# Performance work log

Hardware: AMD Instinct MI355X
Metric: run time of the kernel (lower is better)

## Reference

```python
import jax, jax.numpy as jnp
import numpy as np

B, N, D, E, H = 4, 2048, 512, 16, 1024
CAP = max(4, min(N, int(N * 2.0 / E)))   # eval capacity_factor = 2.0 -> 256
EPS = 1e-9
THRESH = 0.2  # second_threshold_eval


def setup_inputs() -> dict:
    key = jax.random.key(0)
    ks = jax.random.split(key, 10)
    f32 = jnp.float32
    return {
        "X": jax.random.normal(ks[0], (B, N, D), f32),
        "probs": jax.random.uniform(ks[1], (B, N), f32),
        "W1": jax.random.normal(ks[2], (D, D), f32) * (1.0 / np.sqrt(D)),
        "b1": jnp.zeros((D,), f32),
        "Wg": jax.random.normal(ks[3], (D, E), f32),  # Top2Gating uses randn init
        "We1": jax.random.normal(ks[4], (E, D, H), f32) * (1.0 / np.sqrt(D)),
        "We2": jax.random.normal(ks[5], (E, H, D), f32) * (1.0 / np.sqrt(H)),
        "W3": jax.random.normal(ks[6], (D, 4), f32) * (1.0 / np.sqrt(D)),
        "b3": jnp.zeros((4,), f32),
        "W4": jax.random.normal(ks[7], (4, 1), f32) * 0.5,
        "b4": jnp.zeros((1,), f32),
    }


def top2_gating(x, Wg, probs):
    # x: [B, N, D] -> raw gates [B, N, E]
    raw = jax.nn.softmax(jnp.einsum('bnd,de->bne', x, Wg), axis=-1)
    dt = raw.dtype

    gate1 = jnp.max(raw, axis=-1)
    idx1 = jnp.argmax(raw, axis=-1)
    mask1 = jax.nn.one_hot(idx1, E, dtype=dt)
    density_proxy = raw

    raw_wo1 = raw * (1.0 - mask1)
    gate2 = jnp.max(raw_wo1, axis=-1)
    idx2 = jnp.argmax(raw_wo1, axis=-1)
    mask2 = jax.nn.one_hot(idx2, E, dtype=dt)

    denom = gate1 + gate2 + EPS
    gate1 = gate1 / denom
    gate2 = gate2 / denom

    # load-balancing loss (computed but wrapper discards it)
    density1 = jnp.mean(mask1, axis=-2)
    loss = jnp.mean(jnp.mean(density_proxy, axis=-2) * density1) * float(E ** 2)

    # second policy == 'random'
    mask2 = mask2 * (probs < (gate2 / max(THRESH, EPS))).astype(dt)[..., None]

    # exclusive cumsum along the group dim gives position within each expert
    pos1 = (jnp.cumsum(mask1, axis=-2) - mask1) * mask1          # [B, N, E]
    mask1 = mask1 * (pos1 < float(CAP)).astype(dt)
    mask1_count = jnp.sum(mask1, axis=-2, keepdims=True)
    mask1_flat = jnp.sum(mask1, axis=-1)                          # [B, N]
    pos1_flat = jnp.sum(pos1, axis=-1)
    gate1 = gate1 * mask1_flat

    pos2 = ((jnp.cumsum(mask2, axis=-2) - mask2) + mask1_count) * mask2
    mask2 = mask2 * (pos2 < float(CAP)).astype(dt)
    mask2_flat = jnp.sum(mask2, axis=-1)
    pos2_flat = jnp.sum(pos2, axis=-1)
    gate2 = gate2 * mask2_flat

    # safe one-hot: out-of-range positions map to all-zeros (jax.nn.one_hot semantics)
    oh_p1 = jax.nn.one_hot(pos1_flat.astype(jnp.int32), CAP, dtype=dt)
    oh_p2 = jax.nn.one_hot(pos2_flat.astype(jnp.int32), CAP, dtype=dt)
    oh_e1 = jax.nn.one_hot(idx1, E, dtype=dt)
    oh_e2 = jax.nn.one_hot(idx2, E, dtype=dt)

    combine = ((gate1 * mask1_flat)[..., None, None] * oh_e1[..., :, None] * oh_p1[..., None, :]
               + (gate2 * mask2_flat)[..., None, None] * oh_e2[..., :, None] * oh_p2[..., None, :])
    dispatch = (combine != 0).astype(dt)
    return dispatch, combine, loss


def reference(X, probs, W1, b1, Wg, We1, We2, W3, b3, W4, b4):
    h = X @ W1 + b1                                              # linear1
    dispatch, combine, loss = top2_gating(h, Wg, probs)
    exp_in = jnp.einsum('bnd,bnec->ebcd', h, dispatch)           # dispatch
    hid = jax.nn.leaky_relu(jnp.einsum('ebcd,edh->ebch', exp_in, We1))
    exp_out = jnp.einsum('ebch,ehd->ebcd', hid, We2)             # experts
    moe_out = jnp.einsum('bnec,ebcd->bnd', combine, exp_out)     # combine
    out = (moe_out @ W3 + b3) @ W4 + b4                          # hidden3 -> act3
    return out
```

## Files before the change

kernel.cpp:

```cpp
#include <hip/hip_runtime.h>
#include <hip/hip_bf16.h>

#define NB 4
#define NN 2048
#define ND 512
#define NE 16
#define NH 1024
#define CAP 256
#define NTOK (NB*NN)

typedef __attribute__((ext_vector_type(8))) short bf16x8;
typedef __attribute__((ext_vector_type(4))) float f32x4;
typedef __attribute__((ext_vector_type(8))) unsigned short u16x8;

__device__ __forceinline__ void gload16(const void* gsrc, void* lds) {
    __builtin_amdgcn_global_load_lds((const __attribute__((address_space(1))) void*)gsrc,
                                     (__attribute__((address_space(3))) void*)lds, 16, 0, 0);
}
__device__ __forceinline__ unsigned short f2bf(float f) {
    union { __hip_bfloat16 b; unsigned short u; } v; v.b = __float2bfloat16(f); return v.u;
}

__global__ __launch_bounds__(256) void prep_w_kernel(const float* __restrict__ W1,
                                                     const float* __restrict__ Wg,
                                                     unsigned short* __restrict__ W1B,
                                                     float* __restrict__ WcT,
                                                     float* __restrict__ zbuf) {
    const int tid = threadIdx.x;
    int bid = blockIdx.x;
    if (bid < 128) {
        if (bid == 0) zbuf[tid] = 0.f;
        const int w = tid >> 6, l = tid & 63;
        const int d = bid * 4 + w;
        float a0 = 0.f, a1 = 0.f, a2 = 0.f, a3 = 0.f, a4 = 0.f, a5 = 0.f, a6 = 0.f, a7 = 0.f;
        float a8 = 0.f, a9 = 0.f, aA = 0.f, aB = 0.f, aC = 0.f, aD = 0.f, aE = 0.f, aF = 0.f;
        #pragma unroll
        for (int ch = 0; ch < 8; ++ch) {
            float x = W1[(size_t)d * ND + ch * 64 + l];
            const float4* wg4 = (const float4*)(Wg + (size_t)(ch * 64 + l) * NE);
            float4 g0 = wg4[0], g1 = wg4[1], g2 = wg4[2], g3 = wg4[3];
            a0 = fmaf(x, g0.x, a0); a1 = fmaf(x, g0.y, a1); a2 = fmaf(x, g0.z, a2); a3 = fmaf(x, g0.w, a3);
            a4 = fmaf(x, g1.x, a4); a5 = fmaf(x, g1.y, a5); a6 = fmaf(x, g1.z, a6); a7 = fmaf(x, g1.w, a7);
            a8 = fmaf(x, g2.x, a8); a9 = fmaf(x, g2.y, a9); aA = fmaf(x, g2.z, aA); aB = fmaf(x, g2.w, aB);
            aC = fmaf(x, g3.x, aC); aD = fmaf(x, g3.y, aD); aE = fmaf(x, g3.z, aE); aF = fmaf(x, g3.w, aF);
        }
        float accs[16] = {a0, a1, a2, a3, a4, a5, a6, a7, a8, a9, aA, aB, aC, aD, aE, aF};
        #pragma unroll
        for (int off = 32; off >= 1; off >>= 1)
            #pragma unroll
            for (int e = 0; e < 16; ++e) accs[e] += __shfl_xor(accs[e], off);
        #pragma unroll
        for (int e = 0; e < 16; ++e)
            if (l == e) WcT[e * ND + d] = accs[e];
        return;
    }
    bid -= 128;
    {
        int dblk = bid >> 1, hblk = bid & 1;
        const float* src = W1 + (size_t)(dblk * 64) * ND + hblk * 256 + tid;
        unsigned short* dst = W1B + (size_t)(dblk * 512 + hblk * 256 + tid) * 64;
        float v[64];
        #pragma unroll
        for (int j = 0; j < 64; ++j) v[j] = src[(size_t)j * ND];
        #pragma unroll
        for (int q = 0; q < 8; ++q) {
            u16x8 o;
            #pragma unroll
            for (int j = 0; j < 8; ++j) o[j] = f2bf(v[q * 8 + j]);
            *(u16x8*)(dst + q * 8) = o;
        }
    }
}

__global__ __launch_bounds__(256) void gating_stream_kernel(const float* __restrict__ X,
                                                            const float* __restrict__ WcT,
                                                            const float* __restrict__ probs,
                                                            const float* __restrict__ b3,
                                                            const float* __restrict__ W4,
                                                            const float* __restrict__ b4,
                                                            const float* __restrict__ We1,
                                                            unsigned short* __restrict__ Xbf,
                                                            unsigned short* __restrict__ We1B,
                                                            int* __restrict__ idx1a, int* __restrict__ idx2a,
                                                            float* __restrict__ g1a, float* __restrict__ g2a,
                                                            float* __restrict__ out) {
    __shared__ float wc[NE * ND];
    const int tid = threadIdx.x;
    int bid = blockIdx.x;
    const int w = tid >> 6, l = tid & 63;
    if (bid < 512) {
        #pragma unroll
        for (int i = 0; i < 32; ++i) wc[tid + 256 * i] = WcT[tid + 256 * i];
        float c0v = b4[0];
        #pragma unroll
        for (int j = 0; j < 4; ++j) c0v += b3[j] * W4[j];
        __syncthreads();
        const float4* wc4 = (const float4*)wc;
        for (int j = 0; j < 4; ++j) {
            int tok = bid * 16 + j * 4 + w;
            const float4* xrow = (const float4*)(X + (size_t)tok * ND);
            float4 x0 = xrow[l], x1 = xrow[l + 64];
            {
                ushort4 o0, o1;
                o0.x = f2bf(x0.x); o0.y = f2bf(x0.y); o0.z = f2bf(x0.z); o0.w = f2bf(x0.w);
                o1.x = f2bf(x1.x); o1.y = f2bf(x1.y); o1.z = f2bf(x1.z); o1.w = f2bf(x1.w);
                *(ushort4*)(Xbf + (size_t)tok * ND + 4 * l) = o0;
                *(ushort4*)(Xbf + (size_t)tok * ND + 256 + 4 * l) = o1;
            }
            float acc[NE];
            #pragma unroll
            for (int e = 0; e < NE; ++e) {
                float4 w0 = wc4[e * 128 + l], w1 = wc4[e * 128 + l + 64];
                acc[e] = x0.x * w0.x + x0.y * w0.y + x0.z * w0.z + x0.w * w0.w
                       + x1.x * w1.x + x1.y * w1.y + x1.z * w1.z + x1.w * w1.w;
            }
            #pragma unroll
            for (int off = 32; off >= 1; off >>= 1)
                #pragma unroll
                for (int e = 0; e < NE; ++e) acc[e] += __shfl_xor(acc[e], off);

            if (l == 0) {
                float m = acc[0];
                #pragma unroll
                for (int e = 1; e < NE; ++e) m = fmaxf(m, acc[e]);
                float s = 0.f;
                #pragma unroll
                for (int e = 0; e < NE; ++e) { acc[e] = expf(acc[e] - m); s += acc[e]; }
                float inv = 1.f / s;
                #pragma unroll
                for (int e = 0; e < NE; ++e) acc[e] *= inv;
                int i1 = 0; float g1 = acc[0];
                #pragma unroll
                for (int e = 1; e < NE; ++e) if (acc[e] > g1) { g1 = acc[e]; i1 = e; }
                int i2 = -1; float g2 = -1.f;
                #pragma unroll
                for (int e = 0; e < NE; ++e) if (e != i1 && acc[e] > g2) { g2 = acc[e]; i2 = e; }
                float denom = g1 + g2 + 1e-9f;
                float g1n = g1 / denom, g2n = g2 / denom;
                bool flag = probs[tok] < (g2n / 0.2f);
                idx1a[tok] = i1;
                idx2a[tok] = flag ? i2 : -1;
                g1a[tok] = g1n;
                g2a[tok] = g2n;
                out[tok] = c0v;
            }
        }
        return;
    }
    {
        const int unit = bid - 512;
        const int e = unit >> 5, rem = unit & 31;
        const int dblk = rem >> 2, hq = rem & 3;
        const float* src = We1 + (size_t)e * ND * NH + (size_t)(dblk * 64) * NH + hq * 256 + tid;
        unsigned short* dst = We1B + ((size_t)(e * 8 + dblk) * NH + hq * 256 + tid) * 64;
        #pragma unroll
        for (int half = 0; half < 2; ++half) {
            float v[32];
            #pragma unroll
            for (int j = 0; j < 32; ++j) v[j] = src[(size_t)(half * 32 + j) * NH];
            #pragma unroll
            for (int q = 0; q < 4; ++q) {
                u16x8 o;
                #pragma unroll
                for (int j = 0; j < 8; ++j) o[j] = f2bf(v[q * 8 + j]);
                *(u16x8*)(dst + half * 32 + q * 8) = o;
            }
        }
    }
}

__global__ __launch_bounds__(512) void scan_linear1_kernel(const int* __restrict__ idx1a,
                                                           const int* __restrict__ idx2a,
                                                           int* __restrict__ slot_token,
                                                           const unsigned short* __restrict__ Xbf,
                                                           const unsigned short* __restrict__ W1B,
                                                           const float* __restrict__ b1,
                                                           unsigned short* __restrict__ hbf,
                                                           const float* __restrict__ We2,
                                                           const float* __restrict__ W3,
                                                           const float* __restrict__ W4,
                                                           float* __restrict__ u) {
    __shared__ char smem[65536];
    const int tid = threadIdx.x;
    const int w = tid >> 6, l = tid & 63;
    if (blockIdx.x < 64) {
        const int bb = blockIdx.x;
        const int b = bb >> 4, e = bb & 15;
        int* cnt1 = (int*)smem;
        int* cnt2 = cnt1 + 8;
        int* slot = slot_token + (e * NB + b) * CAP;
        const unsigned long long below = (l == 0) ? 0ull : ((1ull << l) - 1ull);
        const int base0 = w * 256;
        int c1 = 0, c2 = 0;
        #pragma unroll
        for (int it = 0; it < 4; ++it) {
            int n = base0 + it * 64 + l;
            c1 += __popcll(__ballot(idx1a[b * NN + n] == e));
            c2 += __popcll(__ballot(idx2a[b * NN + n] == e));
        }
        if (l == 0) { cnt1[w] = c1; cnt2[w] = c2; }
        __syncthreads();
        int b1c = 0, t1 = 0, b2c = 0, t2 = 0;
        #pragma unroll
        for (int i = 0; i < 8; ++i) {
            int v1 = cnt1[i], v2 = cnt2[i];
            if (i < w) { b1c += v1; b2c += v2; }
            t1 += v1; t2 += v2;
        }
        const int start2 = (t1 < CAP) ? t1 : CAP;
        int c = b1c;
        #pragma unroll
        for (int it = 0; it < 4; ++it) {
            int n = base0 + it * 64 + l;
            bool p = (idx1a[b * NN + n] == e);
            unsigned long long m = __ballot(p);
            int pre = __popcll(m & below);
            if (p) { int pos = c + pre; if (pos < CAP) slot[pos] = n; }
            c += __popcll(m);
        }
        c = start2 + b2c;
        #pragma unroll
        for (int it = 0; it < 4; ++it) {
            int n = base0 + it * 64 + l;
            bool p = (idx2a[b * NN + n] == e);
            unsigned long long m = __ballot(p);
            int pre = __popcll(m & below);
            if (p) { int pos = c + pre; if (pos < CAP) slot[pos] = n | (1 << 30); }
            c += __popcll(m);
        }
        int nfill = start2 + t2; nfill = (nfill < CAP) ? nfill : CAP;
        for (int i = nfill + tid; i < CAP; i += 512) slot[i] = -1;
        return;
    }
    if (blockIdx.x < 320) {
        const int lb = blockIdx.x - 64;
        const int m0 = (lb >> 2) * 128, n0 = (lb & 3) * 128;
        const int wm = w >> 1, wn = w & 1;
        const int lr = l & 15, lk = l >> 4;
        char* Ash0 = smem;
        char* Bsh0 = smem + 32768;

        auto stage = [&](int Ks, int buf) {
            #pragma unroll
            for (int i = 0; i < 2; ++i) {
                int o = i * 8192 + tid * 16;
                int r = o >> 7, bb = o & 127;
                int sb2 = bb ^ ((r & 7) << 4);
                gload16((const char*)Xbf + ((size_t)(m0 + r) * ND + Ks * 64) * 2 + sb2,
                        Ash0 + buf * 16384 + i * 8192 + w * 1024);
                gload16((const char*)W1B + ((size_t)(Ks * 512 + n0 + r) * 64) * 2 + sb2,
                        Bsh0 + buf * 16384 + i * 8192 + w * 1024);
            }
        };

        f32x4 acc[2][4] = {};
        stage(0, 0);
        __syncthreads();
        for (int Ks = 0; Ks < 8; ++Ks) {
            int buf = Ks & 1;
            if (Ks < 7) stage(Ks + 1, buf ^ 1);
            #pragma unroll
            for (int k32 = 0; k32 < 2; ++k32) {
                int kb = (k32 * 32 + 8 * lk) * 2;
                bf16x8 a[2], bfr[4];
                #pragma unroll
                for (int mi = 0; mi < 2; ++mi) {
                    int row = wm * 32 + mi * 16 + lr;
                    a[mi] = *(const bf16x8*)(Ash0 + buf * 16384 + row * 128 + (kb ^ ((row & 7) << 4)));
                }
                #pragma unroll
                for (int ni = 0; ni < 4; ++ni) {
                    int row = wn * 64 + ni * 16 + lr;
                    bfr[ni] = *(const bf16x8*)(Bsh0 + buf * 16384 + row * 128 + (kb ^ ((row & 7) << 4)));
                }
                #pragma unroll
                for (int mi = 0; mi < 2; ++mi)
                    #pragma unroll
                    for (int ni = 0; ni < 4; ++ni)
                        acc[mi][ni] = __builtin_amdgcn_mfma_f32_16x16x32_bf16(a[mi], bfr[ni], acc[mi][ni], 0, 0, 0);
            }
            __syncthreads();
        }
        #pragma unroll
        for (int mi = 0; mi < 2; ++mi)
            #pragma unroll
            for (int ni = 0; ni < 4; ++ni) {
                int col = n0 + wn * 64 + ni * 16 + lr;
                float bb1 = b1[col];
                #pragma unroll
                for (int r = 0; r < 4; ++r) {
                    int m = m0 + wm * 32 + mi * 16 + lk * 4 + r;
                    hbf[(size_t)m * ND + col] = f2bf(acc[mi][ni][r] + bb1);
                }
            }
        return;
    }
    {
        const int ub = blockIdx.x - 320;
        float* vvs = (float*)smem;
        {
            float s0 = 0.f;
            #pragma unroll
            for (int j = 0; j < 4; ++j) s0 += W3[tid * 4 + j] * W4[j];
            vvs[tid] = s0;
        }
        __syncthreads();
        const float4* vv4 = (const float4*)vvs;
        const float4 v0 = vv4[l], v1 = vv4[l + 64];
        #pragma unroll
        for (int pass = 0; pass < 4; ++pass) {
            float sums[8];
            #pragma unroll
            for (int i = 0; i < 8; ++i) {
                int gr = ub * 256 + pass * 64 + w * 8 + i;
                const float4* row = (const float4*)(We2 + (size_t)gr * ND);
                float4 a0 = row[l], a1 = row[l + 64];
                sums[i] = a0.x * v0.x + a0.y * v0.y + a0.z * v0.z + a0.w * v0.w
                        + a1.x * v1.x + a1.y * v1.y + a1.z * v1.z + a1.w * v1.w;
            }
            #pragma unroll
            for (int off = 32; off >= 1; off >>= 1)
                #pragma unroll
                for (int i = 0; i < 8; ++i) sums[i] += __shfl_xor(sums[i], off);
            if (l == 0) {
                int gr0 = ub * 256 + pass * 64 + w * 8;
                #pragma unroll
                for (int i = 0; i < 8; ++i) u[gr0 + i] = sums[i];
            }
        }
    }
}

__global__ __launch_bounds__(512) void expert_mfma_kernel(const unsigned short* __restrict__ hbf,
                                                          const unsigned short* __restrict__ We1B,
                                                          const float* __restrict__ u,
                                                          const int* __restrict__ slot_token,
                                                          const float* __restrict__ zbuf,
                                                          const float* __restrict__ g1a,
                                                          const float* __restrict__ g2a,
                                                          float* __restrict__ out) {
    __shared__ char Ash[65536];
    __shared__ char Bsh[2][32768];
    __shared__ float u_lds[NH];
    __shared__ float sbuf[8][64];
    __shared__ int toks[64];
    const int tid = threadIdx.x;
    const int w = tid >> 6, l = tid & 63;
    const int lr = l & 15, lk = l >> 4;
    const int bid = blockIdx.x;
    const int e = (bid & 7) | ((bid >> 7) << 3);
    const int chunk = (bid >> 3) & 15;
    const int b = chunk >> 2, c0 = (chunk & 3) * 64;

    if (tid < 64) toks[tid] = slot_token[(e * NB + b) * CAP + c0 + tid];
    u_lds[tid] = u[e * NH + tid];
    u_lds[tid + 512] = u[e * NH + tid + 512];
    __syncthreads();
    #pragma unroll
    for (int i = 0; i < 8; ++i) {
        int r = i * 8 + w;
        int t = toks[r];
        int tok = t & 2047;
        int sb = (l * 16) ^ ((r & 7) << 4);
        const char* src = (t >= 0) ? ((const char*)hbf + ((size_t)(b * NN + tok) * ND) * 2 + sb)
                                   : ((const char*)zbuf + sb);
        gload16(src, Ash + i * 8192 + w * 1024);
    }
    auto stageB = [&](int s, int buf) {
        int Hc = s >> 4, Ks = s & 15;
        const size_t base = ((size_t)(e * 8 + (Ks >> 1)) * NH + Hc * 512) * 64 + (Ks & 1) * 32;
        #pragma unroll
        for (int i = 0; i < 4; ++i) {
            int r = i * 128 + w * 16 + (l >> 2);
            int swzr = ((r >> 1) & 3) << 4;
            int ebyte = ((l & 3) * 16) ^ swzr;
            gload16((const char*)We1B + (base + (size_t)r * 64) * 2 + ebyte,
                    Bsh[buf] + i * 8192 + w * 1024);
        }
    };
    f32x4 acc[4][4] = {};
    float srow[4][4] = {};
    stageB(0, 0);
    __syncthreads();
    for (int s = 0; s < 32; ++s) {
        int buf = s & 1;
        if (s < 31) stageB(s + 1, buf ^ 1);
        int Ks = s & 15;
        bf16x8 a[4], bb[4];
        #pragma unroll
        for (int mi = 0; mi < 4; ++mi) {
            int row = mi * 16 + lr;
            int kb = (Ks * 64 + lk * 16) ^ ((row & 7) << 4);
            a[mi] = *(const bf16x8*)(Ash + row * 1024 + kb);
        }
        #pragma unroll
        for (int ni = 0; ni < 4; ++ni) {
            int row = w * 64 + ni * 16 + lr;
            int kb = (lk * 16) ^ (((row >> 1) & 3) << 4);
            bb[ni] = *(const bf16x8*)(Bsh[buf] + row * 64 + kb);
        }
        #pragma unroll
        for (int mi = 0; mi < 4; ++mi)
            #pragma unroll
            for (int ni = 0; ni < 4; ++ni)
                acc[mi][ni] = __builtin_amdgcn_mfma_f32_16x16x32_bf16(a[mi], bb[ni], acc[mi][ni], 0, 0, 0);
        if ((s & 15) == 15) {
            int Hc = s >> 4;
            #pragma unroll
            for (int ni = 0; ni < 4; ++ni) {
                float uu = u_lds[Hc * 512 + w * 64 + ni * 16 + lr];
                #pragma unroll
                for (int mi = 0; mi < 4; ++mi)
                    #pragma unroll
                    for (int r = 0; r < 4; ++r) {
                        float x = acc[mi][ni][r];
                        x = (x > 0.f) ? x : 0.01f * x;
                        srow[mi][r] = fmaf(x, uu, srow[mi][r]);
                        acc[mi][ni][r] = 0.f;
                    }
            }
        }
        __syncthreads();
    }
    #pragma unroll
    for (int off = 1; off < 16; off <<= 1)
        #pragma unroll
        for (int mi = 0; mi < 4; ++mi)
            #pragma unroll
            for (int r = 0; r < 4; ++r)
                srow[mi][r] += __shfl_xor(srow[mi][r], off);
    if (lr == 0) {
        #pragma unroll
        for (int mi = 0; mi < 4; ++mi)
            #pragma unroll
            for (int r = 0; r < 4; ++r)
                sbuf[w][mi * 16 + lk * 4 + r] = srow[mi][r];
    }
    __syncthreads();
    if (tid < 64) {
        float s = 0.f;
        #pragma unroll
        for (int q = 0; q < 8; ++q) s += sbuf[q][tid];
        int v = toks[tid];
        if (v >= 0) {
            int tok = v & 2047;
            float g = (v & (1 << 30)) ? g2a[b * NN + tok] : g1a[b * NN + tok];
            atomicAdd(out + b * NN + tok, s * g);
        }
    }
}

extern "C" void kernel_launch(void* const* d_in, const int* in_sizes, int n_in,
                              void* d_out, int out_size, void* d_ws, size_t ws_size,
                              hipStream_t stream) {
    const float* X    = (const float*)d_in[0];
    const float* probs= (const float*)d_in[1];
    const float* W1   = (const float*)d_in[2];
    const float* b1   = (const float*)d_in[3];
    const float* Wg   = (const float*)d_in[4];
    const float* We1  = (const float*)d_in[5];
    const float* We2  = (const float*)d_in[6];
    const float* W3   = (const float*)d_in[7];
    const float* b3   = (const float*)d_in[8];
    const float* W4   = (const float*)d_in[9];
    const float* b4   = (const float*)d_in[10];
    float* out = (float*)d_out;

    char* ws = (char*)d_ws;
    size_t off = 0;
    auto alloc = [&](size_t bytes) { void* p = ws + off; off += (bytes + 255) & ~(size_t)255; return p; };
    unsigned short* Xbf  = (unsigned short*)alloc((size_t)NTOK * ND * 2);
    unsigned short* hbf  = (unsigned short*)alloc((size_t)NTOK * ND * 2);
    unsigned short* W1B  = (unsigned short*)alloc((size_t)ND * ND * 2);
    unsigned short* We1B = (unsigned short*)alloc((size_t)NE * NH * ND * 2);
    float* WcT     = (float*)alloc(NE * ND * 4);
    float* u       = (float*)alloc(NE * NH * 4);
    float* zbuf    = (float*)alloc(1024);
    int*   idx1a   = (int*)alloc(NTOK * 4);
    int*   idx2a   = (int*)alloc(NTOK * 4);
    float* g1a     = (float*)alloc(NTOK * 4);
    float* g2a     = (float*)alloc(NTOK * 4);
    int*   slot_tok= (int*)alloc(NE * NB * CAP * 4);
    (void)ws_size; (void)in_sizes; (void)n_in; (void)out_size;

    prep_w_kernel<<<144, 256, 0, stream>>>(W1, Wg, W1B, WcT, zbuf);
    gating_stream_kernel<<<1024, 256, 0, stream>>>(X, WcT, probs, b3, W4, b4,
                                                   We1, Xbf, We1B,
                                                   idx1a, idx2a, g1a, g2a, out);
    scan_linear1_kernel<<<384, 512, 0, stream>>>(idx1a, idx2a, slot_tok,
                                                 Xbf, W1B, b1, hbf,
                                                 We2, W3, W4, u);
    expert_mfma_kernel<<<256, 512, 0, stream>>>(hbf, We1B, u, slot_tok, zbuf, g1a, g2a, out);
}
```

Baseline: 80.78 us.

## Move We1 bf16 conversion into post kernel and single-buffer linear1 LDS

Moves the We1 fp32-to-bf16 transpose/convert work out of the gating kernel into the following post kernel, where it runs as an extra 512 blocks of 512 threads alongside the scan, linear1 GEMM and We2 reduction blocks. Gating now launches only its 512 token blocks, making it shorter. The linear1 GEMM drops LDS double-buffering to 32KB shared memory with sync before and after each stage, presumably to raise occupancy so the conversion blocks can co-reside. The risk is exposed global-load latency in the GEMM with no prefetch overlap.

After: 81.47 us. No clear change (+0.9%).

```diff
diff --git a/kernel.cpp b/kernel.cpp
--- a/kernel.cpp
+++ b/kernel.cpp
@@ -72,115 +72,92 @@
     }
 }
 
-__global__ __launch_bounds__(256) void gating_stream_kernel(const float* __restrict__ X,
-                                                            const float* __restrict__ WcT,
-                                                            const float* __restrict__ probs,
-                                                            const float* __restrict__ b3,
-                                                            const float* __restrict__ W4,
-                                                            const float* __restrict__ b4,
-                                                            const float* __restrict__ We1,
-                                                            unsigned short* __restrict__ Xbf,
-                                                            unsigned short* __restrict__ We1B,
-                                                            int* __restrict__ idx1a, int* __restrict__ idx2a,
-                                                            float* __restrict__ g1a, float* __restrict__ g2a,
-                                                            float* __restrict__ out) {
+__global__ __launch_bounds__(256) void gating_kernel(const float* __restrict__ X,
+                                                     const float* __restrict__ WcT,
+                                                     const float* __restrict__ probs,
+                                                     const float* __restrict__ b3,
+                                                     const float* __restrict__ W4,
+                                                     const float* __restrict__ b4,
+                                                     unsigned short* __restrict__ Xbf,
+                                                     int* __restrict__ idx1a, int* __restrict__ idx2a,
+                                                     float* __restrict__ g1a, float* __restrict__ g2a,
+                                                     float* __restrict__ out) {
     __shared__ float wc[NE * ND];
     const int tid = threadIdx.x;
-    int bid = blockIdx.x;
+    const int bid = blockIdx.x;
     const int w = tid >> 6, l = tid & 63;
-    if (bid < 512) {
-        #pragma unroll
-        for (int i = 0; i < 32; ++i) wc[tid + 256 * i] = WcT[tid + 256 * i];
-        float c0v = b4[0];
-        #pragma unroll
-        for (int j = 0; j < 4; ++j) c0v += b3[j] * W4[j];
-        __syncthreads();
-        const float4* wc4 = (const float4*)wc;
-        for (int j = 0; j < 4; ++j) {
-            int tok = bid * 16 + j * 4 + w;
-            const float4* xrow = (const float4*)(X + (size_t)tok * ND);
-            float4 x0 = xrow[l], x1 = xrow[l + 64];
-            {
-                ushort4 o0, o1;
-                o0.x = f2bf(x0.x); o0.y = f2bf(x0.y); o0.z = f2bf(x0.z); o0.w = f2bf(x0.w);
-                o1.x = f2bf(x1.x); o1.y = f2bf(x1.y); o1.z = f2bf(x1.z); o1.w = f2bf(x1.w);
-                *(ushort4*)(Xbf + (size_t)tok * ND + 4 * l) = o0;
-                *(ushort4*)(Xbf + (size_t)tok * ND + 256 + 4 * l) = o1;
-            }
-            float acc[NE];
-            #pragma unroll
-            for (int e = 0; e < NE; ++e) {
-                float4 w0 = wc4[e * 128 + l], w1 = wc4[e * 128 + l + 64];
-                acc[e] = x0.x * w0.x + x0.y * w0.y + x0.z * w0.z + x0.w * w0.w
-                       + x1.x * w1.x + x1.y * w1.y + x1.z * w1.z + x1.w * w1.w;
-            }
-            #pragma unroll
-            for (int off = 32; off >= 1; off >>= 1)
-                #pragma unroll
-                for (int e = 0; e < NE; ++e) acc[e] += __shfl_xor(acc[e], off);
-
-            if (l == 0) {
-                float m = acc[0];
-                #pragma unroll
-                for (int e = 1; e < NE; ++e) m = fmaxf(m, acc[e]);
-                float s = 0.f;
-                #pragma unroll
-                for (int e = 0; e < NE; ++e) { acc[e] = expf(acc[e] - m); s += acc[e]; }
-                float inv = 1.f / s;
-                #pragma unroll
-                for (int e = 0; e < NE; ++e) acc[e] *= inv;
-                int i1 = 0; float g1 = acc[0];
-                #pragma unroll
-                for (int e = 1; e < NE; ++e) if (acc[e] > g1) { g1 = acc[e]; i1 = e; }
-                int i2 = -1; float g2 = -1.f;
-                #pragma unroll
-                for (int e = 0; e < NE; ++e) if (e != i1 && acc[e] > g2) { g2 = acc[e]; i2 = e; }
-                float denom = g1 + g2 + 1e-9f;
-                float g1n = g1 / denom, g2n = g2 / denom;
-                bool flag = probs[tok] < (g2n / 0.2f);
-                idx1a[tok] = i1;
-                idx2a[tok] = flag ? i2 : -1;
-                g1a[tok] = g1n;
-                g2a[tok] = g2n;
-                out[tok] = c0v;
-            }
-        }
-        return;
-    }
-    {
-        const int unit = bid - 512;
-        const int e = unit >> 5, rem = unit & 31;
-        const int dblk = rem >> 2, hq = rem & 3;
-        const float* src = We1 + (size_t)e * ND * NH + (size_t)(dblk * 64) * NH + hq * 256 + tid;
-        unsigned short* dst = We1B + ((size_t)(e * 8 + dblk) * NH + hq * 256 + tid) * 64;
-        #pragma unroll
-        for (int half = 0; half < 2; ++half) {
-            float v[32];
-            #pragma unroll
-            for (int j = 0; j < 32; ++j) v[j] = src[(size_t)(half * 32 + j) * NH];
-            #pragma unroll
-            for (int q = 0; q < 4; ++q) {
-                u16x8 o;
-                #pragma unroll
-                for (int j = 0; j < 8; ++j) o[j] = f2bf(v[q * 8 + j]);
-                *(u16x8*)(dst + half * 32 + q * 8) = o;
-            }
-        }
-    }
-}
-
-__global__ __launch_bounds__(512) void scan_linear1_kernel(const int* __restrict__ idx1a,
-                                                           const int* __restrict__ idx2a,
-                                                           int* __restrict__ slot_token,
-                                                           const unsigned short* __restrict__ Xbf,
-                                                           const unsigned short* __restrict__ W1B,
-                                                           const float* __restrict__ b1,
-                                                           unsigned short* __restrict__ hbf,
-                                                           const float* __restrict__ We2,
-                                                           const float* __restrict__ W3,
-                                                           const float* __restrict__ W4,
-                                                           float* __restrict__ u) {
-    __shared__ char smem[65536];
+    #pragma unroll
+    for (int i = 0; i < 32; ++i) wc[tid + 256 * i] = WcT[tid + 256 * i];
+    float c0v = b4[0];
+    #pragma unroll
+    for (int j = 0; j < 4; ++j) c0v += b3[j] * W4[j];
+    __syncthreads();
+    const float4* wc4 = (const float4*)wc;
+    for (int j = 0; j < 4; ++j) {
+        int tok = bid * 16 + j * 4 + w;
+        const float4* xrow = (const float4*)(X + (size_t)tok * ND);
+        float4 x0 = xrow[l], x1 = xrow[l + 64];
+        {
+            ushort4 o0, o1;
+            o0.x = f2bf(x0.x); o0.y = f2bf(x0.y); o0.z = f2bf(x0.z); o0.w = f2bf(x0.w);
+            o1.x = f2bf(x1.x); o1.y = f2bf(x1.y); o1.z = f2bf(x1.z); o1.w = f2bf(x1.w);
+            *(ushort4*)(Xbf + (size_t)tok * ND + 4 * l) = o0;
+            *(ushort4*)(Xbf + (size_t)tok * ND + 256 + 4 * l) = o1;
+        }
+        float acc[NE];
+        #pragma unroll
+        for (int e = 0; e < NE; ++e) {
+            float4 w0 = wc4[e * 128 + l], w1 = wc4[e * 128 + l + 64];
+            acc[e] = x0.x * w0.x + x0.y * w0.y + x0.z * w0.z + x0.w * w0.w
+                   + x1.x * w1.x + x1.y * w1.y + x1.z * w1.z + x1.w * w1.w;
+        }
+        #pragma unroll
+        for (int off = 32; off >= 1; off >>= 1)
+            #pragma unroll
+            for (int e = 0; e < NE; ++e) acc[e] += __shfl_xor(acc[e], off);
+
+        if (l == 0) {
+            float m = acc[0];
+            #pragma unroll
+            for (int e = 1; e < NE; ++e) m = fmaxf(m, acc[e]);
+            float s = 0.f;
+            #pragma unroll
+            for (int e = 0; e < NE; ++e) { acc[e] = expf(acc[e] - m); s += acc[e]; }
+            float inv = 1.f / s;
+            #pragma unroll
+            for (int e = 0; e < NE; ++e) acc[e] *= inv;
+            int i1 = 0; float g1 = acc[0];
+            #pragma unroll
+            for (int e = 1; e < NE; ++e) if (acc[e] > g1) { g1 = acc[e]; i1 = e; }
+            int i2 = -1; float g2 = -1.f;
+            #pragma unroll
+            for (int e = 0; e < NE; ++e) if (e != i1 && acc[e] > g2) { g2 = acc[e]; i2 = e; }
+            float denom = g1 + g2 + 1e-9f;
+            float g1n = g1 / denom, g2n = g2 / denom;
+            bool flag = probs[tok] < (g2n / 0.2f);
+            idx1a[tok] = i1;
+            idx2a[tok] = flag ? i2 : -1;
+            g1a[tok] = g1n;
+            g2a[tok] = g2n;
+            out[tok] = c0v;
+        }
+    }
+}
+
+__global__ __launch_bounds__(512) void post_kernel(const int* __restrict__ idx1a,
+                                                   const int* __restrict__ idx2a,
+                                                   int* __restrict__ slot_token,
+                                                   const unsigned short* __restrict__ Xbf,
+                                                   const unsigned short* __restrict__ W1B,
+                                                   const float* __restrict__ b1,
+                                                   unsigned short* __restrict__ hbf,
+                                                   const float* __restrict__ We1,
+                                                   unsigned short* __restrict__ We1B,
+                                                   const float* __restrict__ We2,
+                                                   const float* __restrict__ W3,
+                                                   const float* __restrict__ W4,
+                                                   float* __restrict__ u) {
+    __shared__ char smem[32768];
     const int tid = threadIdx.x;
     const int w = tid >> 6, l = tid & 63;
     if (blockIdx.x < 64) {
@@ -238,27 +215,28 @@
         const int wm = w >> 1, wn = w & 1;
         const int lr = l & 15, lk = l >> 4;
         char* Ash0 = smem;
-        char* Bsh0 = smem + 32768;
-
-        auto stage = [&](int Ks, int buf) {
-            #pragma unroll
-            for (int i = 0; i < 2; ++i) {
-                int o = i * 8192 + tid * 16;
-                int r = o >> 7, bb = o & 127;
-                int sb2 = bb ^ ((r & 7) << 4);
-                gload16((const char*)Xbf + ((size_t)(m0 + r) * ND + Ks * 64) * 2 + sb2,
-                        Ash0 + buf * 16384 + i * 8192 + w * 1024);
-                gload16((const char*)W1B + ((size_t)(Ks * 512 + n0 + r) * 64) * 2 + sb2,
-                        Bsh0 + buf * 16384 + i * 8192 + w * 1024);
-            }
-        };
+        char* Bsh0 = smem + 16384;
 
         f32x4 acc[2][4] = {};
-        stage(0, 0);
-        __syncthreads();
         for (int Ks = 0; Ks < 8; ++Ks) {
-            int buf = Ks & 1;
-            if (Ks < 7) stage(Ks + 1, buf ^ 1);
+            __syncthreads();
+            {
+                int o = tid * 16;
+                int r0 = o >> 7, bb = o & 127;
+                int sb2 = bb ^ ((r0 & 7) << 4);
+                gload16((const char*)Xbf + ((size_t)(m0 + r0) * ND + Ks * 64) * 2 + sb2,
+                        Ash0 + o);
+                int o2 = o + 8192;
+                int r1 = o2 >> 7;
+                int sb3 = bb ^ ((r1 & 7) << 4);
+                gload16((const char*)Xbf + ((size_t)(m0 + r1) * ND + Ks * 64) * 2 + sb3,
+                        Ash0 + o2);
+                gload16((const char*)W1B + ((size_t)(Ks * 512 + n0 + r0) * 64) * 2 + sb2,
+                        Bsh0 + o);
+                gload16((const char*)W1B + ((size_t)(Ks * 512 + n0 + r1) * 64) * 2 + sb3,
+                        Bsh0 + o2);
+            }
+            __syncthreads();
             #pragma unroll
             for (int k32 = 0; k32 < 2; ++k32) {
                 int kb = (k32 * 32 + 8 * lk) * 2;
@@ -266,12 +244,12 @@
                 #pragma unroll
                 for (int mi = 0; mi < 2; ++mi) {
                     int row = wm * 32 + mi * 16 + lr;
-                    a[mi] = *(const bf16x8*)(Ash0 + buf * 16384 + row * 128 + (kb ^ ((row & 7) << 4)));
+                    a[mi] = *(const bf16x8*)(Ash0 + row * 128 + (kb ^ ((row & 7) << 4)));
                 }
                 #pragma unroll
                 for (int ni = 0; ni < 4; ++ni) {
                     int row = wn * 64 + ni * 16 + lr;
-                    bfr[ni] = *(const bf16x8*)(Bsh0 + buf * 16384 + row * 128 + (kb ^ ((row & 7) << 4)));
+                    bfr[ni] = *(const bf16x8*)(Bsh0 + row * 128 + (kb ^ ((row & 7) << 4)));
                 }
                 #pragma unroll
                 for (int mi = 0; mi < 2; ++mi)
@@ -279,7 +257,6 @@
                     for (int ni = 0; ni < 4; ++ni)
                         acc[mi][ni] = __builtin_amdgcn_mfma_f32_16x16x32_bf16(a[mi], bfr[ni], acc[mi][ni], 0, 0, 0);
             }
-            __syncthreads();
         }
         #pragma unroll
         for (int mi = 0; mi < 2; ++mi)
@@ -295,8 +272,27 @@
             }
         return;
     }
+    if (blockIdx.x < 832) {
+        const int unit = blockIdx.x - 320;
+        const int e = unit >> 5, rem = unit & 31;
+        const int dblk = rem >> 2, hq = rem & 3;
+        const int dhalf = tid >> 8, hl = tid & 255;
+        const float* src = We1 + (size_t)e * ND * NH + (size_t)(dblk * 64 + dhalf * 32) * NH + hq * 256 + hl;
+        unsigned short* dst = We1B + ((size_t)(e * 8 + dblk) * NH + hq * 256 + hl) * 64 + dhalf * 32;
+        float v[32];
+        #pragma unroll
+        for (int j = 0; j < 32; ++j) v[j] = src[(size_t)j * NH];
+        #pragma unroll
+        for (int q = 0; q < 4; ++q) {
+            u16x8 o;
+            #pragma unroll
+            for (int j = 0; j < 8; ++j) o[j] = f2bf(v[q * 8 + j]);
+            *(u16x8*)(dst + q * 8) = o;
+        }
+        return;
+    }
     {
-        const int ub = blockIdx.x - 320;
+        const int ub = blockIdx.x - 832;
         float* vvs = (float*)smem;
         {
             float s0 = 0.f;
@@ -484,11 +480,10 @@
     (void)ws_size; (void)in_sizes; (void)n_in; (void)out_size;
 
     prep_w_kernel<<<144, 256, 0, stream>>>(W1, Wg, W1B, WcT, zbuf);
-    gating_stream_kernel<<<1024, 256, 0, stream>>>(X, WcT, probs, b3, W4, b4,
-                                                   We1, Xbf, We1B,
-                                                   idx1a, idx2a, g1a, g2a, out);
-    scan_linear1_kernel<<<384, 512, 0, stream>>>(idx1a, idx2a, slot_tok,
-                                                 Xbf, W1B, b1, hbf,
-                                                 We2, W3, W4, u);
+    gating_kernel<<<512, 256, 0, stream>>>(X, WcT, probs, b3, W4, b4, Xbf,
+                                           idx1a, idx2a, g1a, g2a, out);
+    post_kernel<<<896, 512, 0, stream>>>(idx1a, idx2a, slot_tok,
+                                         Xbf, W1B, b1, hbf,
+                                         We1, We1B, We2, W3, W4, u);
     expert_mfma_kernel<<<256, 512, 0, stream>>>(hbf, We1B, u, slot_tok, zbuf, g1a, g2a, out);
 }
```
